# Performance work log

Hardware: AMD Instinct MI355X
Metric: run time of the kernel (lower is better)

The kernel has to match this reference:

```python
import jax, jax.numpy as jnp
import numpy as np
import math

B, S = 2, 2048
V, D, H, L, DFF = 1024, 512, 8, 6, 2048
DK = D // H
EPS = 1e-5


def _pos_encoding(seq_len, d_model, dtype):
    pos = jnp.arange(seq_len, dtype=jnp.float32)[:, None]
    div = jnp.exp(jnp.arange(0, d_model, 2, dtype=jnp.float32) * (-math.log(10000.0) / d_model))
    pe = jnp.zeros((seq_len, d_model), dtype=jnp.float32)
    pe = pe.at[:, 0::2].set(jnp.sin(pos * div))
    pe = pe.at[:, 1::2].set(jnp.cos(pos * div))
    return pe.astype(dtype)


def _layernorm(x, w, b):
    mu = jnp.mean(x, axis=-1, keepdims=True)
    var = jnp.mean(jnp.square(x - mu), axis=-1, keepdims=True)
    return (x - mu) * jax.lax.rsqrt(var + EPS) * w + b


def setup_inputs() -> dict:
    key = jax.random.key(0)
    ks = jax.random.split(key, 20)
    s = 0.02
    inp = {
        "input_ids": jax.random.randint(ks[0], (B, S), 1, V),
        "emb": jax.random.normal(ks[1], (V, D)) * s,
        # linear weights stored (in, out) so y = x @ W + b
        "wq": jax.random.normal(ks[2], (L, D, D)) * s,
        "bq": jnp.zeros((L, D)),
        "wk": jax.random.normal(ks[3], (L, D, D)) * s,
        "bk": jnp.zeros((L, D)),
        "wv": jax.random.normal(ks[4], (L, D, D)) * s,
        "bv": jnp.zeros((L, D)),
        "wo": jax.random.normal(ks[5], (L, D, D)) * (s / math.sqrt(2 * L)),
        "bo": jnp.zeros((L, D)),
        "ln1_w": jnp.ones((L, D)), "ln1_b": jnp.zeros((L, D)),
        "ln2_w": jnp.ones((L, D)), "ln2_b": jnp.zeros((L, D)),
        "w1": jax.random.normal(ks[6], (L, D, DFF)) * s,
        "b1": jnp.zeros((L, DFF)),
        "w2": jax.random.normal(ks[7], (L, DFF, D)) * (s / math.sqrt(2 * L)),
        "b2": jnp.zeros((L, D)),
        "out_w": jax.random.normal(ks[8], (D, V)) * s,
        "out_b": jnp.zeros((V,)),
    }
    return inp


def reference(input_ids, emb, wq, bq, wk, bk, wv, bv, wo, bo,
              ln1_w, ln1_b, ln2_w, ln2_b, w1, b1, w2, b2, out_w, out_b):
    pad_mask = (input_ids != 0)                              # [B,S] attend where True
    x = emb[input_ids]                                       # [B,S,D]
    x = x + _pos_encoding(S, D, x.dtype)[None, :, :]
    causal = jnp.tril(jnp.ones((S, S), dtype=bool))          # [S,S]
    mask = causal[None, None, :, :] & pad_mask[:, None, None, :]  # [B,1,S,S]
    scale = 1.0 / math.sqrt(DK)
    for l in range(L):
        h = _layernorm(x, ln1_w[l], ln1_b[l])
        q = (h @ wq[l] + bq[l]).reshape(B, S, H, DK)
        k = (h @ wk[l] + bk[l]).reshape(B, S, H, DK)
        v = (h @ wv[l] + bv[l]).reshape(B, S, H, DK)
        scores = jnp.einsum('bqhd,bkhd->bhqk', q, k) * scale
        scores = jnp.where(mask, scores, -jnp.inf)
        attn = jax.nn.softmax(scores, axis=-1)
        o = jnp.einsum('bhqk,bkhd->bqhd', attn, v).reshape(B, S, D)
        x = o @ wo[l] + bo[l]                                # NOTE: no residual on attention (faithful)
        h2 = _layernorm(x, ln2_w[l], ln2_b[l])
        ff = jax.nn.relu(h2 @ w1[l] + b1[l]) @ w2[l] + b2[l]
        x = x + ff
    logits = x @ out_w + out_b                               # [B,S,V]
    return logits
```

## Files before the change

kernel.cpp:

```cpp
#include <hip/hip_runtime.h>
#include <hip/hip_bf16.h>

#define B_ 2
#define S_ 2048
#define V_ 1024
#define D_ 512
#define H_ 8
#define L_ 6
#define DFF_ 2048
#define DK_ 64
#define MROWS (B_*S_)
#define NEGINF (-__builtin_inff())

typedef __hip_bfloat16 bf16;
typedef __bf16 bf16x8 __attribute__((ext_vector_type(8)));
typedef float f32x4 __attribute__((ext_vector_type(4)));
typedef unsigned short us8 __attribute__((ext_vector_type(8)));
typedef unsigned short us2 __attribute__((ext_vector_type(2)));

__device__ __forceinline__ float bf2f(unsigned short u) {
    return __uint_as_float(((unsigned int)u) << 16);
}
__device__ __forceinline__ unsigned short f2b(float x) {
    unsigned int u = __float_as_uint(x);
    return (unsigned short)((u + 0x7FFFu + ((u >> 16) & 1u)) >> 16);
}
__device__ __forceinline__ float ldin(const void* p, size_t i, int bf) {
    return bf ? bf2f(((const unsigned short*)p)[i]) : ((const float*)p)[i];
}

__device__ __forceinline__ void gload16(const void* g, void* l) {
    __builtin_amdgcn_global_load_lds(
        (const __attribute__((address_space(1))) unsigned int*)g,
        (__attribute__((address_space(3))) unsigned int*)l, 16, 0, 0);
}

__global__ void detect_kernel(const unsigned int* __restrict__ w, int* __restrict__ flag) {
    if (threadIdx.x == 0) flag[0] = (w[0] == 0x3F800000u) ? 0 : 1;
}

__global__ __launch_bounds__(256) void embed_kernel(const int* __restrict__ ids,
        const void* __restrict__ emb, float* __restrict__ x, const int* __restrict__ dtf)
{
    const int bf = dtf[0];
    int tid = blockIdx.x * 256 + threadIdx.x;
    int d = tid % D_;
    int bs = tid / D_;
    int s = bs % S_;
    int id = ids[bs];
    float e = ldin(emb, (size_t)id * D_ + d, bf);
    int i2 = d & ~1;
    float div = expf((float)i2 * (-9.210340371976184f / (float)D_));
    float ang = (float)s * div;
    float pe = (d & 1) ? cosf(ang) : sinf(ang);
    x[tid] = e + pe;
}

__global__ __launch_bounds__(256) void ln_kernel(const float* __restrict__ x,
        const void* __restrict__ w, const void* __restrict__ b, size_t off,
        unsigned short* __restrict__ out, const int* __restrict__ dtf)
{
    const int bf = dtf[0];
    __shared__ float red[256];
    const int row = blockIdx.x;
    const int tid = threadIdx.x;
    const float* xr = x + (size_t)row * D_;
    float v0 = xr[tid], v1 = xr[tid + 256];
    red[tid] = v0 + v1; __syncthreads();
    for (int s = 128; s > 0; s >>= 1) { if (tid < s) red[tid] += red[tid + s]; __syncthreads(); }
    float mu = red[0] * (1.f / D_); __syncthreads();
    float d0 = v0 - mu, d1 = v1 - mu;
    red[tid] = d0 * d0 + d1 * d1; __syncthreads();
    for (int s = 128; s > 0; s >>= 1) { if (tid < s) red[tid] += red[tid + s]; __syncthreads(); }
    float var = red[0] * (1.f / D_);
    float rstd = rsqrtf(var + 1e-5f);
    unsigned short* orow = out + (size_t)row * D_;
    orow[tid]       = f2b(d0 * rstd * ldin(w, off + tid, bf)       + ldin(b, off + tid, bf));
    orow[tid + 256] = f2b(d1 * rstd * ldin(w, off + tid + 256, bf) + ldin(b, off + tid + 256, bf));
}

__device__ __forceinline__ void tr_tile(const void* src, size_t off, int K, int N,
        unsigned short* dst, int k0, int n0, int bf, unsigned short (*T)[72])
{
    const int t = threadIdx.x;
    const int r = t >> 2, c = (t & 3) * 16;
    size_t e = off + (size_t)(k0 + r) * N + n0 + c;
    us8 u0, u1;
    if (bf) {
        u0 = *(const us8*)((const unsigned short*)src + e);
        u1 = *(const us8*)((const unsigned short*)src + e + 8);
    } else {
        const float* p = (const float*)src + e;
        float4 f0 = *(const float4*)p, f1 = *(const float4*)(p + 4);
        float4 f2 = *(const float4*)(p + 8), f3 = *(const float4*)(p + 12);
        u0[0]=f2b(f0.x); u0[1]=f2b(f0.y); u0[2]=f2b(f0.z); u0[3]=f2b(f0.w);
        u0[4]=f2b(f1.x); u0[5]=f2b(f1.y); u0[6]=f2b(f1.z); u0[7]=f2b(f1.w);
        u1[0]=f2b(f2.x); u1[1]=f2b(f2.y); u1[2]=f2b(f2.z); u1[3]=f2b(f2.w);
        u1[4]=f2b(f3.x); u1[5]=f2b(f3.y); u1[6]=f2b(f3.z); u1[7]=f2b(f3.w);
    }
    *(us8*)&T[r][c] = u0;
    *(us8*)&T[r][c + 8] = u1;
    __syncthreads();
    us8 o0, o1;
    #pragma unroll
    for (int i = 0; i < 8; ++i) { o0[i] = T[c + i][r]; o1[i] = T[c + 8 + i][r]; }
    *(us8*)&dst[(size_t)(n0 + r) * K + k0 + c] = o0;
    *(us8*)&dst[(size_t)(n0 + r) * K + k0 + c + 8] = o1;
}

__global__ __launch_bounds__(256) void transpose_all(
        const void* wq, const void* wk, const void* wv, const void* wo,
        const void* w1, const void* w2,
        unsigned short* twq, unsigned short* twk, unsigned short* twv, unsigned short* two,
        unsigned short* tw1, unsigned short* tw2,
        int lbase, int slotmul, const int* __restrict__ dtf)
{
    __shared__ __align__(16) unsigned short T[64][72];
    const int bf = dtf[0];
    const int lrel = blockIdx.x / 768;
    const int within = blockIdx.x % 768;
    const int layer = lbase + lrel;
    const int slot = lrel * slotmul;
    const size_t offQ = (size_t)layer * D_ * D_;
    const size_t offF = (size_t)layer * D_ * DFF_;
    const size_t sQ = (size_t)slot * D_ * D_;
    const size_t sF = (size_t)slot * D_ * DFF_;
    if (within < 256) {
        int sel = within >> 6, tile = within & 63;
        const void* s = sel == 0 ? wq : sel == 1 ? wk : sel == 2 ? wv : wo;
        unsigned short* d = (sel == 0 ? twq : sel == 1 ? twk : sel == 2 ? twv : two) + sQ;
        tr_tile(s, offQ, D_, D_, d, (tile & 7) * 64, (tile >> 3) * 64, bf, T);
    } else if (within < 512) {
        int tile = within - 256;
        tr_tile(w1, offF, D_, DFF_, tw1 + sF, (tile & 7) * 64, (tile >> 3) * 64, bf, T);
    } else {
        int tile = within - 512;
        tr_tile(w2, offF, DFF_, D_, tw2 + sF, (tile & 31) * 64, (tile >> 5) * 64, bf, T);
    }
}

__global__ __launch_bounds__(256) void transpose_one(const void* src, size_t off,
        int K, int N, unsigned short* dst, const int* __restrict__ dtf)
{
    __shared__ __align__(16) unsigned short T[64][72];
    int tile = blockIdx.x;
    int tk = K / 64;
    tr_tile(src, off, K, N, dst, (tile % tk) * 64, (tile / tk) * 64, dtf[0], T);
}

template<int OUTM, bool RELU, bool ADD>
__device__ __forceinline__ void gemm_core128(
        const unsigned short* __restrict__ A, const unsigned short* __restrict__ Wt,
        const void* __restrict__ bias, size_t bOff, const float* __restrict__ Res,
        void* __restrict__ Cout, int M, int N, int K, int bf)
{
    __shared__ __align__(16) unsigned short As[128 * 64];
    __shared__ __align__(16) unsigned short Bs[64 * 64];
    const int tid = threadIdx.x;
    const int wave = tid >> 6, lane = tid & 63;
    const int quad = lane >> 4, l16 = lane & 15;
    const int wm = (wave >> 1) * 64, wn = (wave & 1) * 32;
    const int n0 = blockIdx.x * 64, m0 = blockIdx.y * 128;
    const int arow = tid >> 3, acol = (tid & 7) * 8;

    f32x4 acc[4][2];
    #pragma unroll
    for (int mt = 0; mt < 4; ++mt)
        #pragma unroll
        for (int nt = 0; nt < 2; ++nt)
            acc[mt][nt] = (f32x4){0.f, 0.f, 0.f, 0.f};

    auto stage = [&](int k0) {
        #pragma unroll
        for (int j = 0; j < 4; ++j)
            gload16(A + (size_t)(m0 + j * 32 + arow) * K + k0 + acol,
                    As + j * 2048 + wave * 512);
        #pragma unroll
        for (int j = 0; j < 2; ++j)
            gload16(Wt + (size_t)(n0 + j * 32 + arow) * K + k0 + acol,
                    Bs + j * 2048 + wave * 512);
    };

    stage(0);
    for (int k0 = 0; k0 < K; k0 += 64) {
        __syncthreads();
        bf16x8 af[4][2], bw[2][2];
        #pragma unroll
        for (int mt = 0; mt < 4; ++mt)
            #pragma unroll
            for (int ks = 0; ks < 2; ++ks)
                af[mt][ks] = *(const bf16x8*)&As[(wm + mt * 16 + l16) * 64 + ks * 32 + quad * 8];
        #pragma unroll
        for (int nt = 0; nt < 2; ++nt)
            #pragma unroll
            for (int ks = 0; ks < 2; ++ks)
                bw[nt][ks] = *(const bf16x8*)&Bs[(wn + nt * 16 + l16) * 64 + ks * 32 + quad * 8];
        __syncthreads();
        if (k0 + 64 < K) stage(k0 + 64);
        #pragma unroll
        for (int mt = 0; mt < 4; ++mt)
            #pragma unroll
            for (int nt = 0; nt < 2; ++nt) {
                acc[mt][nt] = __builtin_amdgcn_mfma_f32_16x16x32_bf16(af[mt][0], bw[nt][0], acc[mt][nt], 0, 0, 0);
                acc[mt][nt] = __builtin_amdgcn_mfma_f32_16x16x32_bf16(af[mt][1], bw[nt][1], acc[mt][nt], 0, 0, 0);
            }
    }

    #pragma unroll
    for (int nt = 0; nt < 2; ++nt) {
        int col = n0 + wn + nt * 16 + l16;
        float bv = ldin(bias, bOff + col, bf);
        #pragma unroll
        for (int mt = 0; mt < 4; ++mt) {
            #pragma unroll
            for (int rr = 0; rr < 4; ++rr) {
                int row = m0 + wm + mt * 16 + quad * 4 + rr;
                float c = acc[mt][nt][rr] + bv;
                if (ADD) c += Res[(size_t)row * N + col];
                if (RELU) c = fmaxf(c, 0.f);
                if (OUTM == 0) ((float*)Cout)[(size_t)row * N + col] = c;
                else           ((unsigned short*)Cout)[(size_t)row * N + col] = f2b(c);
            }
        }
    }
}

template<int OUTM, bool RELU, bool ADD>
__global__ __launch_bounds__(256) void gemm128(
        const unsigned short* __restrict__ A, const unsigned short* __restrict__ Wt,
        const void* __restrict__ bias, size_t bOff, const float* __restrict__ Res,
        void* __restrict__ Cout, int M, int N, int K, const int* __restrict__ dtf)
{
    gemm_core128<OUTM, RELU, ADD>(A, Wt, bias, bOff, Res, Cout, M, N, K, dtf[0]);
}

__global__ __launch_bounds__(256) void gemm_qkv128(
        const unsigned short* __restrict__ h,
        const unsigned short* twq, const unsigned short* twk, const unsigned short* twv,
        const void* bq, const void* bk, const void* bv, size_t bOff,
        unsigned short* q, unsigned short* k, unsigned short* v,
        const int* __restrict__ dtf)
{
    const int z = blockIdx.z;
    const unsigned short* W = (z == 0) ? twq : (z == 1) ? twk : twv;
    const void* bias = (z == 0) ? bq : (z == 1) ? bk : bv;
    unsigned short* out = (z == 0) ? q : (z == 1) ? k : v;
    gemm_core128<1, false, false>(h, W, bias, bOff, nullptr, out, MROWS, D_, D_, dtf[0]);
}

template<bool ABF16, int OUTM, bool RELU, bool ADD>
__device__ __forceinline__ void gemm_core64(
        const void* __restrict__ A, const unsigned short* __restrict__ Wt,
        const void* __restrict__ bias, size_t bOff, const float* __restrict__ Res,
        void* __restrict__ Cout, int M, int N, int K, int bf)
{
    __shared__ __align__(16) unsigned short At[64][72];
    __shared__ __align__(16) unsigned short Bt[64][72];
    const int tid = threadIdx.x;
    const int wave = tid >> 6, lane = tid & 63;
    const int quad = lane >> 4, l16 = lane & 15;
    const int wm = (wave >> 1) * 32, wn = (wave & 1) * 32;
    const int n0 = blockIdx.x * 64, m0 = blockIdx.y * 64;
    const int r = tid >> 2, cb = tid & 3;

    f32x4 acc[2][2];
    #pragma unroll
    for (int mt = 0; mt < 2; ++mt)
        #pragma unroll
        for (int nt = 0; nt < 2; ++nt)
            acc[mt][nt] = (f32x4){0.f, 0.f, 0.f, 0.f};

    us8 aR[2], wR[2];
    float4 aF[4];

    auto loadT = [&](int k0) {
        if (ABF16) {
            const unsigned short* Ap = (const unsigned short*)A + (size_t)(m0 + r) * K + k0;
            aR[0] = *(const us8*)(Ap + cb * 8);
            aR[1] = *(const us8*)(Ap + (cb + 4) * 8);
        } else {
            const float* Ap = (const float*)A + (size_t)(m0 + r) * K + k0;
            aF[0] = *(const float4*)(Ap + cb * 8);
            aF[1] = *(const float4*)(Ap + cb * 8 + 4);
            aF[2] = *(const float4*)(Ap + (cb + 4) * 8);
            aF[3] = *(const float4*)(Ap + (cb + 4) * 8 + 4);
        }
        const unsigned short* Wp = Wt + (size_t)(n0 + r) * K + k0;
        wR[0] = *(const us8*)(Wp + cb * 8);
        wR[1] = *(const us8*)(Wp + (cb + 4) * 8);
    };
    auto storeT = [&]() {
        if (ABF16) {
            *(us8*)&At[r][cb * 8] = aR[0];
            *(us8*)&At[r][(cb + 4) * 8] = aR[1];
        } else {
            us8 u0, u1;
            u0[0]=f2b(aF[0].x); u0[1]=f2b(aF[0].y); u0[2]=f2b(aF[0].z); u0[3]=f2b(aF[0].w);
            u0[4]=f2b(aF[1].x); u0[5]=f2b(aF[1].y); u0[6]=f2b(aF[1].z); u0[7]=f2b(aF[1].w);
            u1[0]=f2b(aF[2].x); u1[1]=f2b(aF[2].y); u1[2]=f2b(aF[2].z); u1[3]=f2b(aF[2].w);
            u1[4]=f2b(aF[3].x); u1[5]=f2b(aF[3].y); u1[6]=f2b(aF[3].z); u1[7]=f2b(aF[3].w);
            *(us8*)&At[r][cb * 8] = u0;
            *(us8*)&At[r][(cb + 4) * 8] = u1;
        }
        *(us8*)&Bt[r][cb * 8] = wR[0];
        *(us8*)&Bt[r][(cb + 4) * 8] = wR[1];
    };

    loadT(0);
    for (int k0 = 0; k0 < K; k0 += 64) {
        __syncthreads();
        storeT();
        __syncthreads();
        if (k0 + 64 < K) loadT(k0 + 64);
        bf16x8 af[2][2], bw[2][2];
        #pragma unroll
        for (int mt = 0; mt < 2; ++mt)
            #pragma unroll
            for (int kh = 0; kh < 2; ++kh)
                af[mt][kh] = *(const bf16x8*)&At[wm + mt * 16 + l16][kh * 32 + quad * 8];
        #pragma unroll
        for (int nt = 0; nt < 2; ++nt)
            #pragma unroll
            for (int kh = 0; kh < 2; ++kh)
                bw[nt][kh] = *(const bf16x8*)&Bt[wn + nt * 16 + l16][kh * 32 + quad * 8];
        #pragma unroll
        for (int mt = 0; mt < 2; ++mt)
            #pragma unroll
            for (int nt = 0; nt < 2; ++nt) {
                acc[mt][nt] = __builtin_amdgcn_mfma_f32_16x16x32_bf16(af[mt][0], bw[nt][0], acc[mt][nt], 0, 0, 0);
                acc[mt][nt] = __builtin_amdgcn_mfma_f32_16x16x32_bf16(af[mt][1], bw[nt][1], acc[mt][nt], 0, 0, 0);
            }
    }

    #pragma unroll
    for (int mt = 0; mt < 2; ++mt) {
        #pragma unroll
        for (int nt = 0; nt < 2; ++nt) {
            int col = n0 + wn + nt * 16 + l16;
            float bv = ldin(bias, bOff + col, bf);
            #pragma unroll
            for (int rr = 0; rr < 4; ++rr) {
                int row = m0 + wm + mt * 16 + quad * 4 + rr;
                float c = acc[mt][nt][rr] + bv;
                if (ADD) c += Res[(size_t)row * N + col];
                if (RELU) c = fmaxf(c, 0.f);
                if (OUTM == 0)      ((float*)Cout)[(size_t)row * N + col] = c;
                else if (OUTM == 1) ((unsigned short*)Cout)[(size_t)row * N + col] = f2b(c);
                else {
                    if (bf) ((unsigned short*)Cout)[(size_t)row * N + col] = f2b(c);
                    else    ((float*)Cout)[(size_t)row * N + col] = c;
                }
            }
        }
    }
}

template<bool ABF16, int OUTM, bool RELU, bool ADD>
__global__ __launch_bounds__(256) void gemm64(
        const void* __restrict__ A, const unsigned short* __restrict__ Wt,
        const void* __restrict__ bias, size_t bOff, const float* __restrict__ Res,
        void* __restrict__ Cout, int M, int N, int K, const int* __restrict__ dtf)
{
    gemm_core64<ABF16, OUTM, RELU, ADD>(A, Wt, bias, bOff, Res, Cout, M, N, K, dtf[0]);
}

__global__ __launch_bounds__(512) void attn_flash_v5(
        const unsigned short* __restrict__ qb, const unsigned short* __restrict__ kb,
        const unsigned short* __restrict__ vb, const int* __restrict__ ids,
        unsigned short* __restrict__ ob)
{
    __shared__ __align__(16) unsigned short Qs[2][64][72];
    __shared__ __align__(16) unsigned short Ks[4][64][72];
    __shared__ __align__(16) unsigned short Vt[4][64][72];
    __shared__ __align__(16) unsigned short Ps[2][64][72];
    __shared__ float Msk[S_];
    const int tid = threadIdx.x;
    const int grp = tid >> 8;
    const int t = tid & 255;
    const int wave = t >> 6, lane = t & 63;
    const int quad = lane >> 4, l16 = lane & 15;
    const int p = blockIdx.x, h = blockIdx.y, bz = blockIdx.z;
    const int a = p, bqt = 31 - p;
    const int qt_mine = grp ? bqt : a;
    const size_t hb = (size_t)bz * S_ * D_ + (size_t)h * DK_;
    const int sr = t >> 2, scq = (t & 3) * 16;
    const int pr = t >> 3, cvb = t & 7;

    const int kcols = (bqt + 1) * 64;
    for (int i = tid; i < kcols; i += 512)
        Msk[i] = (ids[bz * S_ + i] == 0) ? NEGINF : 0.f;

    {
        const unsigned short* qp = qb + hb + (size_t)(qt_mine * 64 + sr) * D_ + scq;
        *(us8*)&Qs[grp][sr][scq]     = *(const us8*)qp;
        *(us8*)&Qs[grp][sr][scq + 8] = *(const us8*)(qp + 8);
    }

    us8 kR0, kR1, vA, vB;
    auto loadKV1 = [&](int kt) {
        if (grp == 0) {
            const unsigned short* kp = kb + hb + (size_t)(kt * 64 + sr) * D_ + scq;
            kR0 = *(const us8*)kp;
            kR1 = *(const us8*)(kp + 8);
        } else {
            const unsigned short* vp = vb + hb + (size_t)(kt * 64 + 2 * pr) * D_ + cvb * 8;
            vA = *(const us8*)vp;
            vB = *(const us8*)(vp + D_);
        }
    };
    auto storeKV1 = [&](int buf) {
        if (grp == 0) {
            *(us8*)&Ks[buf][sr][scq]     = kR0;
            *(us8*)&Ks[buf][sr][scq + 8] = kR1;
        } else {
            #pragma unroll
            for (int i = 0; i < 8; ++i) {
                int ii = (i + cvb) & 7;
                us2 u2 = { vA[ii], vB[ii] };
                *(us2*)&Vt[buf][cvb * 8 + ii][2 * pr] = u2;
            }
        }
    };
    auto loadKV2 = [&](int kt) {
        const unsigned short* kp = kb + hb + (size_t)(kt * 64 + sr) * D_ + scq;
        kR0 = *(const us8*)kp;
        kR1 = *(const us8*)(kp + 8);
        const unsigned short* vp = vb + hb + (size_t)(kt * 64 + 2 * pr) * D_ + cvb * 8;
        vA = *(const us8*)vp;
        vB = *(const us8*)(vp + D_);
    };
    auto storeKV2 = [&](int buf) {
        *(us8*)&Ks[buf][sr][scq]     = kR0;
        *(us8*)&Ks[buf][sr][scq + 8] = kR1;
        #pragma unroll
        for (int i = 0; i < 8; ++i) {
            int ii = (i + cvb) & 7;
            us2 u2 = { vA[ii], vB[ii] };
            *(us2*)&Vt[buf][cvb * 8 + ii][2 * pr] = u2;
        }
    };

    f32x4 Oa[4];
    float m[4], l[4];
    #pragma unroll
    for (int r = 0; r < 4; ++r) { m[r] = NEGINF; l[r] = 0.f; }
    #pragma unroll
    for (int dt = 0; dt < 4; ++dt) Oa[dt] = (f32x4){0.f, 0.f, 0.f, 0.f};

    auto stepCompute = [&](int qsel, int kt, int buf, bool causal) {
        f32x4 sa[4];
        #pragma unroll
        for (int nt = 0; nt < 4; ++nt) sa[nt] = (f32x4){0.f, 0.f, 0.f, 0.f};
        #pragma unroll
        for (int ks = 0; ks < 2; ++ks) {
            bf16x8 aq = *(const bf16x8*)&Qs[qsel][wave * 16 + l16][ks * 32 + quad * 8];
            #pragma unroll
            for (int nt = 0; nt < 4; ++nt) {
                bf16x8 bk = *(const bf16x8*)&Ks[buf][nt * 16 + l16][ks * 32 + quad * 8];
                sa[nt] = __builtin_amdgcn_mfma_f32_16x16x32_bf16(aq, bk, sa[nt], 0, 0, 0);
            }
        }
        #pragma unroll
        for (int r = 0; r < 4; ++r) {
            float sv[4];
            #pragma unroll
            for (int nt = 0; nt < 4; ++nt) {
                float s = sa[nt][r] * 0.125f + Msk[kt * 64 + nt * 16 + l16];
                if (causal && (nt * 16 + l16) > (wave * 16 + quad * 4 + r)) s = NEGINF;
                sv[nt] = s;
            }
            float rmax = fmaxf(fmaxf(sv[0], sv[1]), fmaxf(sv[2], sv[3]));
            #pragma unroll
            for (int off = 8; off > 0; off >>= 1)
                rmax = fmaxf(rmax, __shfl_xor(rmax, off, 16));
            float mnew = fmaxf(m[r], rmax);
            float alpha = __expf(m[r] - mnew);
            float pv[4];
            float rsum = 0.f;
            #pragma unroll
            for (int nt = 0; nt < 4; ++nt) { pv[nt] = __expf(sv[nt] - mnew); rsum += pv[nt]; }
            #pragma unroll
            for (int off = 8; off > 0; off >>= 1)
                rsum += __shfl_xor(rsum, off, 16);
            l[r] = l[r] * alpha + rsum;
            m[r] = mnew;
            #pragma unroll
            for (int dt = 0; dt < 4; ++dt) Oa[dt][r] *= alpha;
            int prow = wave * 16 + quad * 4 + r;
            #pragma unroll
            for (int nt = 0; nt < 4; ++nt)
                Ps[grp][prow][nt * 16 + l16] = f2b(pv[nt]);
        }
        #pragma unroll
        for (int ks = 0; ks < 2; ++ks) {
            bf16x8 ap = *(const bf16x8*)&Ps[grp][wave * 16 + l16][ks * 32 + quad * 8];
            #pragma unroll
            for (int dt = 0; dt < 4; ++dt) {
                bf16x8 bv = *(const bf16x8*)&Vt[buf][dt * 16 + l16][ks * 32 + quad * 8];
                Oa[dt] = __builtin_amdgcn_mfma_f32_16x16x32_bf16(ap, bv, Oa[dt], 0, 0, 0);
            }
        }
    };
    auto writeOut = [&](int qt) {
        #pragma unroll
        for (int r = 0; r < 4; ++r) {
            float inv = 1.f / l[r];
            int row = qt * 64 + wave * 16 + quad * 4 + r;
            #pragma unroll
            for (int dt = 0; dt < 4; ++dt)
                ob[hb + (size_t)row * D_ + dt * 16 + l16] = f2b(Oa[dt][r] * inv);
        }
    };

    loadKV1(0);
    storeKV1(0);
    if (a >= 1) loadKV1(1);
    __syncthreads();

    #pragma unroll 1
    for (int kt = 0; kt <= a; ++kt) {
        const int cur = kt & 1;
        stepCompute(grp, kt, cur, kt == qt_mine);
        if (kt + 1 <= a) {
            storeKV1(cur ^ 1);
            if (kt + 2 <= a) loadKV1(kt + 2);
            __syncthreads();
        }
    }
    __syncthreads();

    if (grp == 0) {
        writeOut(a);
        #pragma unroll
        for (int r = 0; r < 4; ++r) { m[r] = NEGINF; l[r] = 0.f; }
        #pragma unroll
        for (int dt = 0; dt < 4; ++dt) Oa[dt] = (f32x4){0.f, 0.f, 0.f, 0.f};
    }

    const int nA = 15 - p, nSteps = 16 - p;
    auto activeP2 = [&](int step) { return grp ? (step < nSteps) : (step < nA); };
    auto ktP2 = [&](int step) { return grp ? (16 + step) : (p + 1 + step); };

    if (activeP2(0)) { loadKV2(ktP2(0)); storeKV2(2 * grp); }
    if (activeP2(1)) loadKV2(ktP2(1));
    __syncthreads();

    #pragma unroll 1
    for (int step = 0; step < nSteps; ++step) {
        if (activeP2(step))
            stepCompute(1, ktP2(step), 2 * grp + (step & 1), ktP2(step) == bqt);
        if (step + 1 < nSteps) {
            if (activeP2(step + 1)) storeKV2(2 * grp + ((step + 1) & 1));
            if (step + 2 < nSteps && activeP2(step + 2)) loadKV2(ktP2(step + 2));
        }
        __syncthreads();
    }

    float* Ob_ = (float*)&Qs[0][0][0];
    float* Ml_ = (float*)&Ps[0][0][0];
    if (grp == 0) {
        #pragma unroll
        for (int r = 0; r < 4; ++r) { Ml_[t * 4 + r] = m[r]; Ml_[1024 + t * 4 + r] = l[r]; }
        #pragma unroll
        for (int dt = 0; dt < 4; ++dt) *(f32x4*)&Ob_[(dt * 256 + t) * 4] = Oa[dt];
    }
    __syncthreads();
    if (grp == 1) {
        #pragma unroll
        for (int r = 0; r < 4; ++r) {
            float mA = Ml_[t * 4 + r], lA = Ml_[1024 + t * 4 + r];
            float mN = fmaxf(m[r], mA);
            float eB = __expf(m[r] - mN), eA = __expf(mA - mN);
            l[r] = l[r] * eB + lA * eA;
            m[r] = mN;
            #pragma unroll
            for (int dt = 0; dt < 4; ++dt)
                Oa[dt][r] = Oa[dt][r] * eB + Ob_[(dt * 256 + t) * 4 + r] * eA;
        }
        writeOut(bqt);
    }
}

extern "C" void kernel_launch(void* const* d_in, const int* in_sizes, int n_in,
                              void* d_out, int out_size, void* d_ws, size_t ws_size,
                              hipStream_t stream)
{
    const int* ids  = (const int*)d_in[0];
    const void* emb = d_in[1];
    const void* wq  = d_in[2];
    const void* bq  = d_in[3];
    const void* wk  = d_in[4];
    const void* bk  = d_in[5];
    const void* wv  = d_in[6];
    const void* bv  = d_in[7];
    const void* wo  = d_in[8];
    const void* bo  = d_in[9];
    const void* ln1w = d_in[10];
    const void* ln1b = d_in[11];
    const void* ln2w = d_in[12];
    const void* ln2b = d_in[13];
    const void* w1  = d_in[14];
    const void* b1  = d_in[15];
    const void* w2  = d_in[16];
    const void* b2  = d_in[17];
    const void* outw = d_in[18];
    const void* outb = d_in[19];

    char* wsp = (char*)d_ws;
    int* dtf = (int*)wsp;
    const size_t NROW = (size_t)MROWS * D_;

    const size_t fixedBytes = 256
        + 2 * NROW * 4
        + 5 * NROW * 2
        + (size_t)MROWS * DFF_ * 2
        + (size_t)D_ * V_ * 2;
    const size_t perLayerW = (4 * (size_t)D_ * D_ + 2 * (size_t)D_ * DFF_) * 2;
    const int slots = (ws_size >= fixedBytes + 6 * perLayerW) ? 6 : 1;

    float* xA = (float*)(wsp + 256);
    float* xB = xA + NROW;
    unsigned short* h  = (unsigned short*)(xB + NROW);
    unsigned short* q  = h + NROW;
    unsigned short* k  = q + NROW;
    unsigned short* v  = k + NROW;
    unsigned short* o  = v + NROW;
    unsigned short* ff = o + NROW;
    unsigned short* twout = ff + (size_t)MROWS * DFF_;
    unsigned short* twq = twout + (size_t)D_ * V_;
    unsigned short* twk = twq + (size_t)slots * D_ * D_;
    unsigned short* twv = twk + (size_t)slots * D_ * D_;
    unsigned short* two = twv + (size_t)slots * D_ * D_;
    unsigned short* tw1 = two + (size_t)slots * D_ * D_;
    unsigned short* tw2 = tw1 + (size_t)slots * D_ * DFF_;

    detect_kernel<<<1, 64, 0, stream>>>((const unsigned int*)ln1w, dtf);
    transpose_one<<<(D_/64) * (V_/64), 256, 0, stream>>>(outw, 0, D_, V_, twout, dtf);
    if (slots == 6)
        transpose_all<<<6 * 768, 256, 0, stream>>>(wq, wk, wv, wo, w1, w2,
            twq, twk, twv, two, tw1, tw2, 0, 1, dtf);
    embed_kernel<<<(MROWS * D_) / 256, 256, 0, stream>>>(ids, emb, xA, dtf);

    for (int l = 0; l < L_; ++l) {
        const size_t bOff = (size_t)l * D_;
        const int s = (slots == 6) ? l : 0;
        if (slots == 1)
            transpose_all<<<768, 256, 0, stream>>>(wq, wk, wv, wo, w1, w2,
                twq, twk, twv, two, tw1, tw2, l, 0, dtf);
        const unsigned short* lwq = twq + (size_t)s * D_ * D_;
        const unsigned short* lwk = twk + (size_t)s * D_ * D_;
        const unsigned short* lwv = twv + (size_t)s * D_ * D_;
        const unsigned short* lwo = two + (size_t)s * D_ * D_;
        const unsigned short* lw1 = tw1 + (size_t)s * D_ * DFF_;
        const unsigned short* lw2 = tw2 + (size_t)s * D_ * DFF_;

        ln_kernel<<<MROWS, 256, 0, stream>>>(xA, ln1w, ln1b, bOff, h, dtf);
        gemm_qkv128<<<dim3(D_/64, MROWS/128, 3), 256, 0, stream>>>(
            h, lwq, lwk, lwv, bq, bk, bv, bOff, q, k, v, dtf);
        attn_flash_v5<<<dim3(S_/128, H_, B_), 512, 0, stream>>>(q, k, v, ids, o);
        gemm128<0, false, false><<<dim3(D_/64, MROWS/128), 256, 0, stream>>>(
            o, lwo, bo, bOff, nullptr, xB, MROWS, D_, D_, dtf);
        ln_kernel<<<MROWS, 256, 0, stream>>>(xB, ln2w, ln2b, bOff, h, dtf);
        gemm128<1, true, false><<<dim3(DFF_/64, MROWS/128), 256, 0, stream>>>(
            h, lw1, b1, (size_t)l * DFF_, nullptr, ff, MROWS, DFF_, D_, dtf);
        gemm128<0, false, true><<<dim3(D_/64, MROWS/128), 256, 0, stream>>>(
            ff, lw2, b2, bOff, xB, xA, MROWS, D_, DFF_, dtf);
    }
    gemm64<false, 2, false, false><<<dim3(V_/64, MROWS/64), 256, 0, stream>>>(
        xA, twout, outb, 0, nullptr, d_out, MROWS, V_, D_, dtf);
}
```

Baseline: 1.129 ms.

## Double-buffer LDS GEMM with XOR swizzle and 64x64 tiles

Reworks the shared LDS GEMM core used for QKV, output projection and both FFN matmuls. The block tile shrinks from 128x64 to 64x64, which doubles the grid. LDS is double-buffered so the next K-slice load is issued right after one barrier instead of two. An XOR swizzle on LDS columns is meant to avoid bank conflicts on the bf16x8 fragment reads. The smaller tile lowers per-block reuse of B-weights, traded for more blocks in flight and fewer syncs.

Measured after the change: 1.063 ms. 1.06x faster.

```diff
diff --git a/kernel.cpp b/kernel.cpp
--- a/kernel.cpp
+++ b/kernel.cpp
@@ -149,69 +149,75 @@
 }
 
 template<int OUTM, bool RELU, bool ADD>
-__device__ __forceinline__ void gemm_core128(
+__device__ __forceinline__ void gemm_core_lds(
         const unsigned short* __restrict__ A, const unsigned short* __restrict__ Wt,
         const void* __restrict__ bias, size_t bOff, const float* __restrict__ Res,
         void* __restrict__ Cout, int M, int N, int K, int bf)
 {
-    __shared__ __align__(16) unsigned short As[128 * 64];
-    __shared__ __align__(16) unsigned short Bs[64 * 64];
+    __shared__ __align__(16) unsigned short As[2][64 * 64];
+    __shared__ __align__(16) unsigned short Bs[2][64 * 64];
     const int tid = threadIdx.x;
     const int wave = tid >> 6, lane = tid & 63;
     const int quad = lane >> 4, l16 = lane & 15;
-    const int wm = (wave >> 1) * 64, wn = (wave & 1) * 32;
-    const int n0 = blockIdx.x * 64, m0 = blockIdx.y * 128;
-    const int arow = tid >> 3, acol = (tid & 7) * 8;
-
-    f32x4 acc[4][2];
+    const int wm = (wave >> 1) * 32, wn = (wave & 1) * 32;
+    const int n0 = blockIdx.x * 64, m0 = blockIdx.y * 64;
+    const int srow = lane >> 3;
+    const int scol = 8 * ((lane & 7) ^ (lane >> 3));
+
+    f32x4 acc[2][2];
     #pragma unroll
-    for (int mt = 0; mt < 4; ++mt)
+    for (int mt = 0; mt < 2; ++mt)
         #pragma unroll
         for (int nt = 0; nt < 2; ++nt)
             acc[mt][nt] = (f32x4){0.f, 0.f, 0.f, 0.f};
 
-    auto stage = [&](int k0) {
-        #pragma unroll
-        for (int j = 0; j < 4; ++j)
-            gload16(A + (size_t)(m0 + j * 32 + arow) * K + k0 + acol,
-                    As + j * 2048 + wave * 512);
-        #pragma unroll
-        for (int j = 0; j < 2; ++j)
-            gload16(Wt + (size_t)(n0 + j * 32 + arow) * K + k0 + acol,
-                    Bs + j * 2048 + wave * 512);
-    };
-
-    stage(0);
+    auto stage = [&](int k0, int buf) {
+        #pragma unroll
+        for (int j = 0; j < 2; ++j) {
+            int row = (wave * 2 + j) * 8 + srow;
+            gload16(A  + (size_t)(m0 + row) * K + k0 + scol, &As[buf][(wave * 2 + j) * 512]);
+            gload16(Wt + (size_t)(n0 + row) * K + k0 + scol, &Bs[buf][(wave * 2 + j) * 512]);
+        }
+    };
+
+    stage(0, 0);
+    int cur = 0;
     for (int k0 = 0; k0 < K; k0 += 64) {
         __syncthreads();
-        bf16x8 af[4][2], bw[2][2];
-        #pragma unroll
-        for (int mt = 0; mt < 4; ++mt)
-            #pragma unroll
-            for (int ks = 0; ks < 2; ++ks)
-                af[mt][ks] = *(const bf16x8*)&As[(wm + mt * 16 + l16) * 64 + ks * 32 + quad * 8];
+        if (k0 + 64 < K) stage(k0 + 64, cur ^ 1);
+        bf16x8 af[2][2], bw[2][2];
+        #pragma unroll
+        for (int mt = 0; mt < 2; ++mt)
+            #pragma unroll
+            for (int ks = 0; ks < 2; ++ks) {
+                int row = wm + mt * 16 + l16;
+                int cs = ks * 32 + quad * 8;
+                af[mt][ks] = *(const bf16x8*)&As[cur][row * 64 + (cs ^ ((row & 7) * 8))];
+            }
         #pragma unroll
         for (int nt = 0; nt < 2; ++nt)
             #pragma unroll
-            for (int ks = 0; ks < 2; ++ks)
-                bw[nt][ks] = *(const bf16x8*)&Bs[(wn + nt * 16 + l16) * 64 + ks * 32 + quad * 8];
-        __syncthreads();
-        if (k0 + 64 < K) stage(k0 + 64);
-        #pragma unroll
-        for (int mt = 0; mt < 4; ++mt)
+            for (int ks = 0; ks < 2; ++ks) {
+                int row = wn + nt * 16 + l16;
+                int cs = ks * 32 + quad * 8;
+                bw[nt][ks] = *(const bf16x8*)&Bs[cur][row * 64 + (cs ^ ((row & 7) * 8))];
+            }
+        #pragma unroll
+        for (int mt = 0; mt < 2; ++mt)
             #pragma unroll
             for (int nt = 0; nt < 2; ++nt) {
                 acc[mt][nt] = __builtin_amdgcn_mfma_f32_16x16x32_bf16(af[mt][0], bw[nt][0], acc[mt][nt], 0, 0, 0);
                 acc[mt][nt] = __builtin_amdgcn_mfma_f32_16x16x32_bf16(af[mt][1], bw[nt][1], acc[mt][nt], 0, 0, 0);
             }
+        cur ^= 1;
     }
 
     #pragma unroll
-    for (int nt = 0; nt < 2; ++nt) {
-        int col = n0 + wn + nt * 16 + l16;
-        float bv = ldin(bias, bOff + col, bf);
-        #pragma unroll
-        for (int mt = 0; mt < 4; ++mt) {
+    for (int mt = 0; mt < 2; ++mt) {
+        #pragma unroll
+        for (int nt = 0; nt < 2; ++nt) {
+            int col = n0 + wn + nt * 16 + l16;
+            float bv = ldin(bias, bOff + col, bf);
             #pragma unroll
             for (int rr = 0; rr < 4; ++rr) {
                 int row = m0 + wm + mt * 16 + quad * 4 + rr;
@@ -226,15 +232,15 @@
 }
 
 template<int OUTM, bool RELU, bool ADD>
-__global__ __launch_bounds__(256) void gemm128(
+__global__ __launch_bounds__(256) void gemm_lds(
         const unsigned short* __restrict__ A, const unsigned short* __restrict__ Wt,
         const void* __restrict__ bias, size_t bOff, const float* __restrict__ Res,
         void* __restrict__ Cout, int M, int N, int K, const int* __restrict__ dtf)
 {
-    gemm_core128<OUTM, RELU, ADD>(A, Wt, bias, bOff, Res, Cout, M, N, K, dtf[0]);
-}
-
-__global__ __launch_bounds__(256) void gemm_qkv128(
+    gemm_core_lds<OUTM, RELU, ADD>(A, Wt, bias, bOff, Res, Cout, M, N, K, dtf[0]);
+}
+
+__global__ __launch_bounds__(256) void gemm_qkv_lds(
         const unsigned short* __restrict__ h,
         const unsigned short* twq, const unsigned short* twk, const unsigned short* twv,
         const void* bq, const void* bk, const void* bv, size_t bOff,
@@ -245,7 +251,7 @@
     const unsigned short* W = (z == 0) ? twq : (z == 1) ? twk : twv;
     const void* bias = (z == 0) ? bq : (z == 1) ? bk : bv;
     unsigned short* out = (z == 0) ? q : (z == 1) ? k : v;
-    gemm_core128<1, false, false>(h, W, bias, bOff, nullptr, out, MROWS, D_, D_, dtf[0]);
+    gemm_core_lds<1, false, false>(h, W, bias, bOff, nullptr, out, MROWS, D_, D_, dtf[0]);
 }
 
 template<bool ABF16, int OUTM, bool RELU, bool ADD>
@@ -655,15 +661,15 @@
         const unsigned short* lw2 = tw2 + (size_t)s * D_ * DFF_;
 
         ln_kernel<<<MROWS, 256, 0, stream>>>(xA, ln1w, ln1b, bOff, h, dtf);
-        gemm_qkv128<<<dim3(D_/64, MROWS/128, 3), 256, 0, stream>>>(
+        gemm_qkv_lds<<<dim3(D_/64, MROWS/64, 3), 256, 0, stream>>>(
             h, lwq, lwk, lwv, bq, bk, bv, bOff, q, k, v, dtf);
         attn_flash_v5<<<dim3(S_/128, H_, B_), 512, 0, stream>>>(q, k, v, ids, o);
-        gemm128<0, false, false><<<dim3(D_/64, MROWS/128), 256, 0, stream>>>(
+        gemm_lds<0, false, false><<<dim3(D_/64, MROWS/64), 256, 0, stream>>>(
             o, lwo, bo, bOff, nullptr, xB, MROWS, D_, D_, dtf);
         ln_kernel<<<MROWS, 256, 0, stream>>>(xB, ln2w, ln2b, bOff, h, dtf);
-        gemm128<1, true, false><<<dim3(DFF_/64, MROWS/128), 256, 0, stream>>>(
+        gemm_lds<1, true, false><<<dim3(DFF_/64, MROWS/64), 256, 0, stream>>>(
             h, lw1, b1, (size_t)l * DFF_, nullptr, ff, MROWS, DFF_, D_, dtf);
-        gemm128<0, false, true><<<dim3(D_/64, MROWS/128), 256, 0, stream>>>(
+        gemm_lds<0, false, true><<<dim3(D_/64, MROWS/64), 256, 0, stream>>>(
             ff, lw2, b2, bOff, xB, xA, MROWS, D_, DFF_, dtf);
     }
     gemm64<false, 2, false, false><<<dim3(V_/64, MROWS/64), 256, 0, stream>>>(
```
